# Performance work log

Hardware: AMD Instinct MI355X
Metric: run time of the kernel (lower is better)

The kernel has to match this reference:

```python
import jax, jax.numpy as jnp
import numpy as np

BN_EPS = 1e-5


def cond_conv(x, att_w, att_b, weight, pad):
    """CondConv: per-sample expert-mixed conv.
    x: [N,C,H,W]; att_w: [K,C]; att_b: [K]; weight: [K,O,I,kh,kw]; pad: (ph,pw)."""
    pooled = x.mean(axis=(2, 3))                         # [N,C]  (AdaptiveAvgPool2d(1))
    att = jax.nn.sigmoid(pooled @ att_w.T + att_b)       # [N,K]  (1x1 conv + sigmoid)
    agg_w = jnp.einsum('nk,koihw->noihw', att, weight)   # per-sample kernels [N,O,I,kh,kw]

    def conv1(xi, wi):
        return jax.lax.conv_general_dilated(
            xi[None], wi, window_strides=(1, 1),
            padding=[(pad[0], pad[0]), (pad[1], pad[1])],
            dimension_numbers=('NCHW', 'OIHW', 'NCHW'))[0]

    return jax.vmap(conv1)(x, agg_w)                     # [N,O,H,W]


def batchnorm(x, gamma, beta):
    # training-mode BN: biased batch stats over (N,H,W)
    mean = x.mean(axis=(0, 2, 3), keepdims=True)
    var = x.var(axis=(0, 2, 3), keepdims=True)
    xn = (x - mean) * jax.lax.rsqrt(var + BN_EPS)
    return xn * gamma[None, :, None, None] + beta[None, :, None, None]


def channel_shuffle(x, g):
    N, C, H, W = x.shape
    return x.reshape(N, g, C // g, H, W).transpose(0, 2, 1, 3, 4).reshape(N, C, H, W)


def setup_inputs() -> dict:
    key = jax.random.key(0)
    ks = jax.random.split(key, 8)
    N, C, H, W = 32, 256, 64, 64
    Cb, K = C // 4, 4
    inp = {
        'x': jax.random.normal(ks[0], (N, C, H, W), jnp.float32),
        'sq_att_w': jax.random.normal(ks[1], (K, Cb), jnp.float32) * 0.1,
        'sq_att_b': jnp.zeros((K,), jnp.float32),
        'sq_w': jax.random.normal(ks[2], (K, Cb, Cb, 3, 3), jnp.float32) * 0.05,
        'sq_g': jnp.ones((Cb,), jnp.float32),
        'sq_b': jnp.zeros((Cb,), jnp.float32),
        'ver_att_w': jax.random.normal(ks[3], (K, Cb), jnp.float32) * 0.1,
        'ver_att_b': jnp.zeros((K,), jnp.float32),
        'ver_w': jax.random.normal(ks[4], (K, Cb, Cb, 3, 1), jnp.float32) * 0.05,
        'ver_g': jnp.ones((Cb,), jnp.float32),
        'ver_b': jnp.zeros((Cb,), jnp.float32),
        'hor_att_w': jax.random.normal(ks[5], (K, Cb), jnp.float32) * 0.1,
        'hor_att_b': jnp.zeros((K,), jnp.float32),
        'hor_w': jax.random.normal(ks[6], (K, Cb, Cb, 1, 3), jnp.float32) * 0.05,
        'hor_g': jnp.ones((Cb,), jnp.float32),
        'hor_b': jnp.zeros((Cb,), jnp.float32),
    }
    return inp


def reference(x, sq_att_w, sq_att_b, sq_w, sq_g, sq_b,
              ver_att_w, ver_att_b, ver_w, ver_g, ver_b,
              hor_att_w, hor_att_b, hor_w, hor_g, hor_b):
    # q_Split: chunk into 4 along channels
    s0, s1, s2, s3 = jnp.split(x, 4, axis=1)
    # square branch: CondConv 3x3 pad 1 + BN
    sq = batchnorm(cond_conv(s1, sq_att_w, sq_att_b, sq_w, (1, 1)), sq_g, sq_b)
    # vertical branch: CondConv 3x1 pad (1,0) + BN (crop layer is Identity since offset=0)
    ve = batchnorm(cond_conv(s2, ver_att_w, ver_att_b, ver_w, (1, 0)), ver_g, ver_b)
    # horizontal branch: CondConv 1x3 pad (0,1) + BN
    ho = batchnorm(cond_conv(s3, hor_att_w, hor_att_b, hor_w, (0, 1)), hor_g, hor_b)
    out = jnp.concatenate((s0, sq, ve, ho), axis=1)
    return channel_shuffle(out, 8)
```

## Files before the change

kernel.cpp:

```cpp
#include <hip/hip_runtime.h>
#include <cstddef>
#include <cstdint>


typedef __attribute__((ext_vector_type(8))) short frag8;
typedef __attribute__((ext_vector_type(16))) float accf16;

#define HW 4096
#define CNT_INV (1.0f / 131072.0f)
#define CSTR 1056
#define RSTR 8448
#define XT_BR (32ull * 66 * 8448)

#define WS_POOLED 0
#define WS_ATT    6144
#define WS_SS     6528
#define WS_PST    6912
#define WS_WBF_SQ  203520
#define WS_WBF_VER 793344
#define WS_WBF_HOR 989952
#define WS_XT      1186560

__device__ __forceinline__ int shuf_ch(int c) { return ((c & 31) << 3) | (c >> 5); }

__device__ __forceinline__ unsigned bf16pair(float a, float b) {
    unsigned ua = __builtin_bit_cast(unsigned, a);
    unsigned ub = __builtin_bit_cast(unsigned, b);
    ua = (ua + 0x7fffu + ((ua >> 16) & 1u)) >> 16;
    ub = (ub + 0x7fffu + ((ub >> 16) & 1u)) >> 16;
    return ua | (ub << 16);
}

__device__ __forceinline__ void gload_lds16(const void* g, void* l) {
    __builtin_amdgcn_global_load_lds(
        (const __attribute__((address_space(1))) void*)g,
        (__attribute__((address_space(3))) void*)l, 16, 0, 0);
}

__global__ void __launch_bounds__(256) prepass_kernel(
    const float* __restrict__ x, unsigned char* __restrict__ xt,
    float* __restrict__ pooled) {
    const int bid = blockIdx.x;
    const int c8 = bid & 7;
    const int n = (bid >> 3) & 31;
    const int b = bid >> 8;
    const int tid = threadIdx.x;
    const int w = tid & 63, q = tid >> 6;
    const float* xb = x + (size_t)(n * 256 + 64 * (b + 1) + c8 * 8) * HW;
    unsigned char* xtb = xt + (size_t)b * XT_BR + (size_t)n * 66 * RSTR + c8 * CSTR;

    float ps[8] = {0.f, 0.f, 0.f, 0.f, 0.f, 0.f, 0.f, 0.f};
    for (int h = q; h < 64; h += 4) {
        float v[8];
#pragma unroll
        for (int j = 0; j < 8; ++j) v[j] = xb[(size_t)j * HW + h * 64 + w];
        unsigned pk[4];
#pragma unroll
        for (int j = 0; j < 4; ++j) pk[j] = bf16pair(v[2 * j], v[2 * j + 1]);
        *(uint4*)(xtb + (size_t)(h + 1) * RSTR + (w + 1) * 16) = *(uint4*)pk;
#pragma unroll
        for (int j = 0; j < 8; ++j) ps[j] += v[j];
    }
    for (int idx = tid; idx < 260; idx += 256) {
        int p, slot;
        if (idx < 66)       { p = 0;         slot = idx; }
        else if (idx < 132) { p = 65;        slot = idx - 66; }
        else if (idx < 196) { p = idx - 131; slot = 0; }
        else                { p = idx - 195; slot = 65; }
        *(uint4*)(xtb + (size_t)p * RSTR + slot * 16) = uint4{0, 0, 0, 0};
    }
    __shared__ float red[4][8];
#pragma unroll
    for (int j = 0; j < 8; ++j)
#pragma unroll
        for (int off = 32; off; off >>= 1) ps[j] += __shfl_down(ps[j], off, 64);
    if ((tid & 63) == 0)
#pragma unroll
        for (int j = 0; j < 8; ++j) red[q][j] = ps[j];
    __syncthreads();
    if (tid < 8)
        pooled[(b * 32 + n) * 64 + c8 * 8 + tid] =
            (red[0][tid] + red[1][tid] + red[2][tid] + red[3][tid]) * (1.f / 4096.f);
}

__global__ void __launch_bounds__(64) att_all_kernel(
    const float* __restrict__ pooled,
    const float* __restrict__ aw0, const float* __restrict__ ab0,
    const float* __restrict__ aw1, const float* __restrict__ ab1,
    const float* __restrict__ aw2, const float* __restrict__ ab2,
    float* __restrict__ att) {
    int bid = blockIdx.x;
    int b = bid >> 5;
    const float* aw = (b == 0) ? aw0 : (b == 1) ? aw1 : aw2;
    const float* ab = (b == 0) ? ab0 : (b == 1) ? ab1 : ab2;
    int t = threadIdx.x;
    float p = pooled[bid * 64 + t];
#pragma unroll
    for (int k = 0; k < 4; ++k) {
        float v = p * aw[k * 64 + t];
#pragma unroll
        for (int off = 32; off; off >>= 1) v += __shfl_down(v, off, 64);
        if (t == 0) att[bid * 4 + k] = 1.f / (1.f + expf(-(v + ab[k])));
    }
}

template <int TAPS>
__device__ __forceinline__ void aggbf_body(const float* __restrict__ w,
                                           const float* __restrict__ att,
                                           unsigned* __restrict__ wbf, int bid) {
    int idx = bid * 256 + threadIdx.x;
    int ip = idx & 31;
    int o  = (idx >> 5) & 63;
    int t  = (idx >> 11) % TAPS;
    int n  = (idx >> 11) / TAPS;
    const float* a = att + n * 4;
    constexpr int PS = 64 * 64 * TAPS;
    int base = (o * 64 + ip * 2) * TAPS + t;
    float v0 = a[0]*w[base] + a[1]*w[PS+base] + a[2]*w[2*PS+base] + a[3]*w[3*PS+base];
    int base1 = base + TAPS;
    float v1 = a[0]*w[base1] + a[1]*w[PS+base1] + a[2]*w[2*PS+base1] + a[3]*w[3*PS+base1];
    wbf[idx] = bf16pair(v0, v1);
}

__global__ void __launch_bounds__(256) aggbf_all_kernel(
    const float* __restrict__ sq_w, const float* __restrict__ ver_w,
    const float* __restrict__ hor_w, const float* __restrict__ att,
    unsigned* __restrict__ wsq, unsigned* __restrict__ wver,
    unsigned* __restrict__ whor) {
    int bid = blockIdx.x;
    if (bid < 2304)      aggbf_body<9>(sq_w,  att,       wsq,  bid);
    else if (bid < 3072) aggbf_body<3>(ver_w, att + 128, wver, bid - 2304);
    else                 aggbf_body<3>(hor_w, att + 256, whor, bid - 3072);
}

template <int KH, int KW, int PH, int PW>
__device__ __forceinline__ void conv_body(
    const unsigned char* __restrict__ xt, const unsigned* __restrict__ wbf,
    float* __restrict__ out, float* __restrict__ pst, int cbase, int bid,
    unsigned char* xs, float (*red1)[2][2][16], float (*red2)[2][2][16]) {
    constexpr int TAPS = KH * KW;
    constexpr int HB = 4;
    constexpr int ROWS = HB + KH - 1;
    constexpr int TOT = ROWS * RSTR;
    constexpr int NCH = (TOT + 1023) >> 10;
    const int hb = bid & 15, n = bid >> 4;
    const int h0 = hb * HB;
    const int tid = threadIdx.x;
    const int lane = tid & 63;
    const int wv = tid >> 6;
    const int rh = wv >> 1, wn = wv & 1;
    const int l31 = lane & 31, hi = lane >> 5;
    const int wcol = wn * 32 + l31;

    {
        const unsigned char* src = xt +
            (size_t)(n * 66 + h0 + (KH == 1 ? 1 : 0)) * RSTR + lane * 16;
#pragma unroll
        for (int c = wv; c < NCH; c += 4)
            gload_lds16(src + (c << 10), xs + (c << 10));
    }

    const frag8* wp = (const frag8*)wbf + ((size_t)n * TAPS * 64 + l31) * 8 + hi;

    __syncthreads();

    accf16 a00 = {}, a01 = {}, a10 = {}, a11 = {};
#pragma unroll
    for (int t = 0; t < TAPS; ++t) {
        const int r_ = t / KW, dw = t % KW - PW;
        frag8 af[8];
#pragma unroll
        for (int kk = 0; kk < 4; ++kk) {
            af[kk]     = wp[t * 512 + kk * 2];
            af[4 + kk] = wp[t * 512 + 256 + kk * 2];
        }
        const unsigned char* bp = xs + (rh * 2 + r_) * RSTR + hi * CSTR +
                                  (wcol + dw + 1) * 16;
#pragma unroll
        for (int kk = 0; kk < 4; ++kk) {
            frag8 b0 = *(const frag8*)(bp + kk * 2 * CSTR);
            frag8 b1 = *(const frag8*)(bp + kk * 2 * CSTR + RSTR);
            a00 = __builtin_amdgcn_mfma_f32_32x32x16_bf16(af[kk],     b0, a00, 0, 0, 0);
            a10 = __builtin_amdgcn_mfma_f32_32x32x16_bf16(af[4 + kk], b0, a10, 0, 0, 0);
            a01 = __builtin_amdgcn_mfma_f32_32x32x16_bf16(af[kk],     b1, a01, 0, 0, 0);
            a11 = __builtin_amdgcn_mfma_f32_32x32x16_bf16(af[4 + kk], b1, a11, 0, 0, 0);
        }
    }

    {
        float* ob = out + (size_t)n * 256 * HW + (h0 + rh * 2) * 64 + wcol;
#pragma unroll
        for (int rg = 0; rg < 16; ++rg) {
            const int o = (rg & 3) + 8 * (rg >> 2) + 4 * hi;
            float* p0 = ob + (size_t)shuf_ch(cbase + o) * HW;
            p0[0]  = a00[rg];
            p0[64] = a01[rg];
            float* p1 = ob + (size_t)shuf_ch(cbase + 32 + o) * HW;
            p1[0]  = a10[rg];
            p1[64] = a11[rg];
        }
    }

#pragma unroll
    for (int rg = 0; rg < 16; ++rg) {
        float u1 = a00[rg] + a01[rg];
        float u2 = a00[rg] * a00[rg] + a01[rg] * a01[rg];
        float w1 = a10[rg] + a11[rg];
        float w2 = a10[rg] * a10[rg] + a11[rg] * a11[rg];
#pragma unroll
        for (int off = 16; off; off >>= 1) {
            u1 += __shfl_down(u1, off, 32);
            u2 += __shfl_down(u2, off, 32);
            w1 += __shfl_down(w1, off, 32);
            w2 += __shfl_down(w2, off, 32);
        }
        if (l31 == 0) {
            red1[wv][0][hi][rg] = u1; red2[wv][0][hi][rg] = u2;
            red1[wv][1][hi][rg] = w1; red2[wv][1][hi][rg] = w2;
        }
    }
    __syncthreads();
    if (tid < 64) {
        const int rg = tid & 15, hi2 = (tid >> 4) & 1, wm2 = tid >> 5;
        float s1 = 0.f, s2 = 0.f;
#pragma unroll
        for (int v = 0; v < 4; ++v) {
            s1 += red1[v][wm2][hi2][rg];
            s2 += red2[v][wm2][hi2][rg];
        }
        const int o = wm2 * 32 + (rg & 3) + 8 * (rg >> 2) + 4 * hi2;
        const int slot = n * 16 + hb;
        pst[o * 1024 + slot] = s1;
        pst[o * 1024 + 512 + slot] = s2;
    }
}

__device__ __forceinline__ void s0_body(const float* __restrict__ x,
                                        float* __restrict__ out, int bid) {
    const int n = bid >> 4, c0 = (bid & 15) * 4, tid = threadIdx.x;
#pragma unroll
    for (int j = 0; j < 4; ++j) {
        const int c = c0 + j;
        const float4* s = (const float4*)(x + (size_t)(n * 256 + c) * HW);
        float4* d = (float4*)(out + (size_t)(n * 256 + shuf_ch(c)) * HW);
#pragma unroll
        for (int it = 0; it < 4; ++it) d[tid + it * 256] = s[tid + it * 256];
    }
}

__global__ void __launch_bounds__(256, 3) conv_all_kernel(
    const float* __restrict__ x, const unsigned char* __restrict__ xt,
    const unsigned* __restrict__ wsq, const unsigned* __restrict__ wver,
    const unsigned* __restrict__ whor,
    float* __restrict__ out, float* __restrict__ pst) {
    __shared__ __align__(16) unsigned char xs[6 * RSTR + 512];
    __shared__ float red1[4][2][2][16], red2[4][2][2][16];
    int bid = blockIdx.x;
    if (bid < 512)
        conv_body<3, 3, 1, 1>(xt, wsq, out, pst, 64, bid, xs, red1, red2);
    else if (bid < 1024)
        conv_body<3, 1, 1, 0>(xt + XT_BR, wver, out, pst + 65536, 128,
                              bid - 512, xs, red1, red2);
    else if (bid < 1536)
        conv_body<1, 3, 0, 1>(xt + 2 * XT_BR, whor, out, pst + 131072, 192,
                              bid - 1024, xs, red1, red2);
    else
        s0_body(x, out, bid - 1536);
}

__global__ void __launch_bounds__(256) bnstats_all_kernel(
    const float* __restrict__ pst,
    const float* __restrict__ g0, const float* __restrict__ b0,
    const float* __restrict__ g1, const float* __restrict__ b1,
    const float* __restrict__ g2, const float* __restrict__ b2,
    float* __restrict__ ss) {
    int br = blockIdx.x >> 6, o = blockIdx.x & 63, t = threadIdx.x;
    const float* gamma = (br == 0) ? g0 : (br == 1) ? g1 : g2;
    const float* beta  = (br == 0) ? b0 : (br == 1) ? b1 : b2;
    const float* p = pst + br * 65536 + o * 1024;
    float s1 = 0.f, s2 = 0.f;
    for (int i = t; i < 512; i += 256) {
        s1 += p[i];
        s2 += p[512 + i];
    }
#pragma unroll
    for (int off = 32; off; off >>= 1) {
        s1 += __shfl_down(s1, off, 64);
        s2 += __shfl_down(s2, off, 64);
    }
    __shared__ float r1[4], r2[4];
    if ((t & 63) == 0) { r1[t >> 6] = s1; r2[t >> 6] = s2; }
    __syncthreads();
    if (t == 0) {
        float S1 = r1[0] + r1[1] + r1[2] + r1[3];
        float S2 = r2[0] + r2[1] + r2[2] + r2[3];
        float mean = S1 * CNT_INV;
        float var = S2 * CNT_INV - mean * mean;
        float scale = rsqrtf(var + 1e-5f) * gamma[o];
        ss[br * 128 + o * 2 + 0] = scale;
        ss[br * 128 + o * 2 + 1] = beta[o] - mean * scale;
    }
}

__global__ void __launch_bounds__(256) bn_all_kernel(float* __restrict__ out,
                                                     const float* __restrict__ ss) {
    int gbid = blockIdx.x;
    int sub = gbid >> 13;
    int bid = gbid & 8191;
    int chunk = bid & 3;
    int n = (bid >> 2) & 31;
    int o = bid >> 7;
    float scale = ss[sub * 128 + o * 2], shift = ss[sub * 128 + o * 2 + 1];
    int c_out = shuf_ch(64 * (sub + 1) + o);
    float4* p = (float4*)(out + (size_t)(n * 256 + c_out) * HW) + chunk * 256 + threadIdx.x;
    float4 v = *p;
    v.x = fmaf(v.x, scale, shift);
    v.y = fmaf(v.y, scale, shift);
    v.z = fmaf(v.z, scale, shift);
    v.w = fmaf(v.w, scale, shift);
    *p = v;
}

extern "C" void kernel_launch(void* const* d_in, const int* in_sizes, int n_in,
                              void* d_out, int out_size, void* d_ws, size_t ws_size,
                              hipStream_t stream) {
    const float* x        = (const float*)d_in[0];
    const float* sq_att_w = (const float*)d_in[1];
    const float* sq_att_b = (const float*)d_in[2];
    const float* sq_w     = (const float*)d_in[3];
    const float* sq_g     = (const float*)d_in[4];
    const float* sq_b     = (const float*)d_in[5];
    const float* ver_att_w= (const float*)d_in[6];
    const float* ver_att_b= (const float*)d_in[7];
    const float* ver_w    = (const float*)d_in[8];
    const float* ver_g    = (const float*)d_in[9];
    const float* ver_b    = (const float*)d_in[10];
    const float* hor_att_w= (const float*)d_in[11];
    const float* hor_att_b= (const float*)d_in[12];
    const float* hor_w    = (const float*)d_in[13];
    const float* hor_g    = (const float*)d_in[14];
    const float* hor_b    = (const float*)d_in[15];
    float* out = (float*)d_out;
    float* ws = (float*)d_ws;

    float* pooled = ws + WS_POOLED;
    float* att    = ws + WS_ATT;
    float* ss     = ws + WS_SS;
    float* pst    = ws + WS_PST;
    unsigned* wbf_sq  = (unsigned*)(ws + WS_WBF_SQ);
    unsigned* wbf_ver = (unsigned*)(ws + WS_WBF_VER);
    unsigned* wbf_hor = (unsigned*)(ws + WS_WBF_HOR);
    unsigned char* xt = (unsigned char*)(ws + WS_XT);

    prepass_kernel<<<768, 256, 0, stream>>>(x, xt, pooled);
    att_all_kernel<<<96, 64, 0, stream>>>(pooled, sq_att_w, sq_att_b,
                                          ver_att_w, ver_att_b,
                                          hor_att_w, hor_att_b, att);
    aggbf_all_kernel<<<3840, 256, 0, stream>>>(sq_w, ver_w, hor_w, att,
                                               wbf_sq, wbf_ver, wbf_hor);
    conv_all_kernel<<<2048, 256, 0, stream>>>(x, xt, wbf_sq, wbf_ver, wbf_hor,
                                              out, pst);
    bnstats_all_kernel<<<192, 256, 0, stream>>>(pst, sq_g, sq_b, ver_g, ver_b,
                                                hor_g, hor_b, ss);
    bn_all_kernel<<<24576, 256, 0, stream>>>(out, ss);
}
```

Measured before the change: 163.2 us.

## Fuse attention into weight aggregation, relayout bf16 weights, double-buffer A loads

Removes the separate attention kernel launch. Each aggregation block now recomputes its sample's sigmoid attention from the pooled means in shared memory. The bf16 aggregated weight layout is changed so each lane's fragment loads are contiguous across lanes, which should give coalesced global reads in the conv. The conv tap loop now ping-pongs two register fragment buffers so the next tap's weights are prefetched while the current MFMAs run. The trade-offs are redundant attention math per block and higher register pressure.

```diff
diff --git a/kernel.cpp b/kernel.cpp
--- a/kernel.cpp
+++ b/kernel.cpp
@@ -13,7 +13,6 @@
 #define XT_BR (32ull * 66 * 8448)
 
 #define WS_POOLED 0
-#define WS_ATT    6144
 #define WS_SS     6528
 #define WS_PST    6912
 #define WS_WBF_SQ  203520
@@ -83,55 +82,78 @@
             (red[0][tid] + red[1][tid] + red[2][tid] + red[3][tid]) * (1.f / 4096.f);
 }
 
-__global__ void __launch_bounds__(64) att_all_kernel(
+template <int TAPS>
+__device__ __forceinline__ void aggbf_body(const float* __restrict__ w,
+                                           const float* __restrict__ pooled_b,
+                                           const float* __restrict__ aw,
+                                           const float* __restrict__ ab,
+                                           unsigned* __restrict__ wbf, int bid) {
+    const int tid = threadIdx.x;
+    int idx = bid * 256 + tid;
+    int ip = idx & 31;
+    int o  = (idx >> 5) & 63;
+    int t  = (idx >> 11) % TAPS;
+    int n  = (idx >> 11) / TAPS;
+
+    __shared__ float satt[4];
+    if (tid < 64) {
+        float p = pooled_b[n * 64 + tid];
+#pragma unroll
+        for (int k = 0; k < 4; ++k) {
+            float v = p * aw[k * 64 + tid];
+#pragma unroll
+            for (int off = 32; off; off >>= 1) v += __shfl_down(v, off, 64);
+            if (tid == 0) satt[k] = 1.f / (1.f + expf(-(v + ab[k])));
+        }
+    }
+    __syncthreads();
+    const float a0 = satt[0], a1 = satt[1], a2 = satt[2], a3 = satt[3];
+
+    constexpr int PS = 64 * 64 * TAPS;
+    int base = (o * 64 + ip * 2) * TAPS + t;
+    float v0 = a0*w[base] + a1*w[PS+base] + a2*w[2*PS+base] + a3*w[3*PS+base];
+    int base1 = base + TAPS;
+    float v1 = a0*w[base1] + a1*w[PS+base1] + a2*w[2*PS+base1] + a3*w[3*PS+base1];
+    int f = ip >> 2, jj = ip & 3;
+    wbf[(((n * TAPS + t) * 8 + f) * 64 + o) * 4 + jj] = bf16pair(v0, v1);
+}
+
+__global__ void __launch_bounds__(256) aggbf_all_kernel(
     const float* __restrict__ pooled,
     const float* __restrict__ aw0, const float* __restrict__ ab0,
     const float* __restrict__ aw1, const float* __restrict__ ab1,
     const float* __restrict__ aw2, const float* __restrict__ ab2,
-    float* __restrict__ att) {
-    int bid = blockIdx.x;
-    int b = bid >> 5;
-    const float* aw = (b == 0) ? aw0 : (b == 1) ? aw1 : aw2;
-    const float* ab = (b == 0) ? ab0 : (b == 1) ? ab1 : ab2;
-    int t = threadIdx.x;
-    float p = pooled[bid * 64 + t];
-#pragma unroll
-    for (int k = 0; k < 4; ++k) {
-        float v = p * aw[k * 64 + t];
-#pragma unroll
-        for (int off = 32; off; off >>= 1) v += __shfl_down(v, off, 64);
-        if (t == 0) att[bid * 4 + k] = 1.f / (1.f + expf(-(v + ab[k])));
-    }
-}
-
-template <int TAPS>
-__device__ __forceinline__ void aggbf_body(const float* __restrict__ w,
-                                           const float* __restrict__ att,
-                                           unsigned* __restrict__ wbf, int bid) {
-    int idx = bid * 256 + threadIdx.x;
-    int ip = idx & 31;
-    int o  = (idx >> 5) & 63;
-    int t  = (idx >> 11) % TAPS;
-    int n  = (idx >> 11) / TAPS;
-    const float* a = att + n * 4;
-    constexpr int PS = 64 * 64 * TAPS;
-    int base = (o * 64 + ip * 2) * TAPS + t;
-    float v0 = a[0]*w[base] + a[1]*w[PS+base] + a[2]*w[2*PS+base] + a[3]*w[3*PS+base];
-    int base1 = base + TAPS;
-    float v1 = a[0]*w[base1] + a[1]*w[PS+base1] + a[2]*w[2*PS+base1] + a[3]*w[3*PS+base1];
-    wbf[idx] = bf16pair(v0, v1);
-}
-
-__global__ void __launch_bounds__(256) aggbf_all_kernel(
     const float* __restrict__ sq_w, const float* __restrict__ ver_w,
-    const float* __restrict__ hor_w, const float* __restrict__ att,
+    const float* __restrict__ hor_w,
     unsigned* __restrict__ wsq, unsigned* __restrict__ wver,
     unsigned* __restrict__ whor) {
     int bid = blockIdx.x;
-    if (bid < 2304)      aggbf_body<9>(sq_w,  att,       wsq,  bid);
-    else if (bid < 3072) aggbf_body<3>(ver_w, att + 128, wver, bid - 2304);
-    else                 aggbf_body<3>(hor_w, att + 256, whor, bid - 3072);
-}
+    if (bid < 2304)
+        aggbf_body<9>(sq_w, pooled, aw0, ab0, wsq, bid);
+    else if (bid < 3072)
+        aggbf_body<3>(ver_w, pooled + 2048, aw1, ab1, wver, bid - 2304);
+    else
+        aggbf_body<3>(hor_w, pooled + 4096, aw2, ab2, whor, bid - 3072);
+}
+
+#define LOADA(dst, tt) \
+    _Pragma("unroll") for (int kk = 0; kk < 4; ++kk) { \
+        dst[kk]     = wp[(tt) * 512 + kk * 128]; \
+        dst[4 + kk] = wp[(tt) * 512 + kk * 128 + 32]; \
+    }
+
+#define TAPSTEP(tt, CUR) { \
+    const int r_ = (tt) / KW, dw_ = (tt) % KW - PW; \
+    const unsigned char* bp_ = xs + (rh * 2 + r_) * RSTR + hi * CSTR + \
+                               (wcol + dw_ + 1) * 16; \
+    _Pragma("unroll") for (int kk = 0; kk < 4; ++kk) { \
+        frag8 b0 = *(const frag8*)(bp_ + kk * 2 * CSTR); \
+        frag8 b1 = *(const frag8*)(bp_ + kk * 2 * CSTR + RSTR); \
+        a00 = __builtin_amdgcn_mfma_f32_32x32x16_bf16(CUR[kk],     b0, a00, 0, 0, 0); \
+        a10 = __builtin_amdgcn_mfma_f32_32x32x16_bf16(CUR[4 + kk], b0, a10, 0, 0, 0); \
+        a01 = __builtin_amdgcn_mfma_f32_32x32x16_bf16(CUR[kk],     b1, a01, 0, 0, 0); \
+        a11 = __builtin_amdgcn_mfma_f32_32x32x16_bf16(CUR[4 + kk], b1, a11, 0, 0, 0); \
+    } }
 
 template <int KH, int KW, int PH, int PW>
 __device__ __forceinline__ void conv_body(
@@ -160,31 +182,19 @@
             gload_lds16(src + (c << 10), xs + (c << 10));
     }
 
-    const frag8* wp = (const frag8*)wbf + ((size_t)n * TAPS * 64 + l31) * 8 + hi;
-
+    const frag8* wp = (const frag8*)wbf + (size_t)n * TAPS * 512 + hi * 64 + l31;
+
+    frag8 aA[8], aB[8];
+    LOADA(aA, 0);
     __syncthreads();
 
     accf16 a00 = {}, a01 = {}, a10 = {}, a11 = {};
 #pragma unroll
-    for (int t = 0; t < TAPS; ++t) {
-        const int r_ = t / KW, dw = t % KW - PW;
-        frag8 af[8];
-#pragma unroll
-        for (int kk = 0; kk < 4; ++kk) {
-            af[kk]     = wp[t * 512 + kk * 2];
-            af[4 + kk] = wp[t * 512 + 256 + kk * 2];
-        }
-        const unsigned char* bp = xs + (rh * 2 + r_) * RSTR + hi * CSTR +
-                                  (wcol + dw + 1) * 16;
-#pragma unroll
-        for (int kk = 0; kk < 4; ++kk) {
-            frag8 b0 = *(const frag8*)(bp + kk * 2 * CSTR);
-            frag8 b1 = *(const frag8*)(bp + kk * 2 * CSTR + RSTR);
-            a00 = __builtin_amdgcn_mfma_f32_32x32x16_bf16(af[kk],     b0, a00, 0, 0, 0);
-            a10 = __builtin_amdgcn_mfma_f32_32x32x16_bf16(af[4 + kk], b0, a10, 0, 0, 0);
-            a01 = __builtin_amdgcn_mfma_f32_32x32x16_bf16(af[kk],     b1, a01, 0, 0, 0);
-            a11 = __builtin_amdgcn_mfma_f32_32x32x16_bf16(af[4 + kk], b1, a11, 0, 0, 0);
-        }
+    for (int t = 0; t < TAPS; t += 2) {
+        if (t + 1 < TAPS) LOADA(aB, t + 1);
+        TAPSTEP(t, aA);
+        if (t + 2 < TAPS) LOADA(aA, t + 2);
+        if (t + 1 < TAPS) TAPSTEP(t + 1, aB);
     }
 
     {
@@ -344,7 +354,6 @@
     float* ws = (float*)d_ws;
 
     float* pooled = ws + WS_POOLED;
-    float* att    = ws + WS_ATT;
     float* ss     = ws + WS_SS;
     float* pst    = ws + WS_PST;
     unsigned* wbf_sq  = (unsigned*)(ws + WS_WBF_SQ);
@@ -353,10 +362,11 @@
     unsigned char* xt = (unsigned char*)(ws + WS_XT);
 
     prepass_kernel<<<768, 256, 0, stream>>>(x, xt, pooled);
-    att_all_kernel<<<96, 64, 0, stream>>>(pooled, sq_att_w, sq_att_b,
-                                          ver_att_w, ver_att_b,
-                                          hor_att_w, hor_att_b, att);
-    aggbf_all_kernel<<<3840, 256, 0, stream>>>(sq_w, ver_w, hor_w, att,
+    aggbf_all_kernel<<<3840, 256, 0, stream>>>(pooled,
+                                               sq_att_w, sq_att_b,
+                                               ver_att_w, ver_att_b,
+                                               hor_att_w, hor_att_b,
+                                               sq_w, ver_w, hor_w,
                                                wbf_sq, wbf_ver, wbf_hor);
     conv_all_kernel<<<2048, 256, 0, stream>>>(x, xt, wbf_sq, wbf_ver, wbf_hor,
                                               out, pst);
```

Measured after the change: 156.2 us. 4.3% less time.
